# Performance work log

Measured on AMD Instinct MI355X. Metric: run time of the kernel, lower is better.

## Reference

```python
import jax, jax.numpy as jnp
import numpy as np

WS = 7        # window size (cubic)
SHIFT = 3     # shift size (cubic)
NH = 6        # num heads
EPS = 1e-5


def _layernorm(x, g, b):
    m = x.mean(-1, keepdims=True)
    v = ((x - m) ** 2).mean(-1, keepdims=True)
    return (x - m) / jnp.sqrt(v + EPS) * g + b


def _win_partition(x, ws):
    # (B,H,W,T,C) -> (B*nW, ws^3, C)
    B, H, W, T, C = x.shape
    x = x.reshape(B, H // ws, ws, W // ws, ws, T // ws, ws, C)
    return x.transpose(0, 1, 3, 5, 2, 4, 6, 7).reshape(-1, ws * ws * ws, C)


def _win_reverse(w, ws, B, H, W, T):
    # (B*nW, ws^3, C) -> (B,H,W,T,C)
    C = w.shape[-1]
    x = w.reshape(B, H // ws, W // ws, T // ws, ws, ws, ws, C)
    return x.transpose(0, 1, 4, 2, 5, 3, 6, 7).reshape(B, H, W, T, C)


def _rel_index(ws):
    # 3D relative position index, (N, N) int, N = ws^3 (torch.meshgrid default 'ij')
    coords = np.stack(np.meshgrid(np.arange(ws), np.arange(ws), np.arange(ws), indexing='ij'))
    cf = coords.reshape(3, -1)
    rel = (cf[:, :, None] - cf[:, None, :]).transpose(1, 2, 0)
    rel[:, :, 0] += ws - 1
    rel[:, :, 1] += ws - 1
    rel[:, :, 2] += ws - 1
    rel[:, :, 0] *= (2 * ws - 1) ** 2
    rel[:, :, 1] *= (2 * ws - 1)
    return rel.sum(-1)


def _compute_mask(Hp, Wp, Tp, ws, shift):
    img = np.zeros((1, Hp, Wp, Tp, 1), np.float32)
    cnt = 0
    sl = (slice(0, -ws), slice(-ws, -shift), slice(-shift, None))
    for h in sl:
        for w in sl:
            for t in sl:
                img[:, h, w, t, :] = cnt
                cnt += 1
    mw = np.asarray(_win_partition(jnp.asarray(img), ws)).reshape(-1, ws ** 3)  # (nW, N)
    am = mw[:, None, :] - mw[:, :, None]
    return jnp.asarray(np.where(am != 0, -100.0, 0.0).astype(np.float32))


def setup_inputs() -> dict:
    key = jax.random.key(0)
    ks = jax.random.split(key, 10)
    B, Hd, Wd, Td, C = 2, 28, 28, 28, 192
    L = Hd * Wd * Td
    Ch = int(C * 4.0)
    s = 0.02
    inp = {
        'x': jax.random.normal(ks[0], (B, L, C), jnp.float32),
        'mask': _compute_mask(Hd, Wd, Td, WS, SHIFT),
        'gamma1': jnp.ones((C,), jnp.float32),
        'beta1': jnp.zeros((C,), jnp.float32),
        'qkv_w': jax.random.normal(ks[1], (3 * C, C), jnp.float32) * s,
        'qkv_b': jnp.zeros((3 * C,), jnp.float32),
        'rpb_table': jax.random.normal(ks[2], ((2 * WS - 1) ** 3, NH), jnp.float32) * s,
        'proj_w': jax.random.normal(ks[3], (C, C), jnp.float32) * s,
        'proj_b': jnp.zeros((C,), jnp.float32),
        'gamma2': jnp.ones((C,), jnp.float32),
        'beta2': jnp.zeros((C,), jnp.float32),
        'fc1_w': jax.random.normal(ks[4], (Ch, C), jnp.float32) * s,
        'fc1_b': jnp.zeros((Ch,), jnp.float32),
        'fc2_w': jax.random.normal(ks[5], (C, Ch), jnp.float32) * s,
        'fc2_b': jnp.zeros((C,), jnp.float32),
        'H': Hd, 'W': Wd, 'T': Td,
    }
    return inp


def reference(x, mask, gamma1, beta1, qkv_w, qkv_b, rpb_table, proj_w, proj_b,
              gamma2, beta2, fc1_w, fc1_b, fc2_w, fc2_b, H, W, T):
    B, L, C = x.shape
    hd = C // NH
    scale = hd ** -0.5
    shortcut = x

    h1 = _layernorm(x, gamma1, beta1).reshape(B, H, W, T, C)
    # H,W,T are multiples of WS -> no padding; cyclic shift for SW-MSA
    shifted = jnp.roll(h1, (-SHIFT, -SHIFT, -SHIFT), axis=(1, 2, 3))
    xw = _win_partition(shifted, WS)            # (B*nW, N, C)
    Bn, N, _ = xw.shape

    qkv = (xw @ qkv_w.T + qkv_b).reshape(Bn, N, 3, NH, hd).transpose(2, 0, 3, 1, 4)
    q, k, v = qkv[0] * scale, qkv[1], qkv[2]     # (Bn, NH, N, hd)
    attn = jnp.einsum('bhnd,bhmd->bhnm', q, k)   # (Bn, NH, N, N)

    idx = _rel_index(WS)
    bias = rpb_table[idx.reshape(-1)].reshape(N, N, NH).transpose(2, 0, 1)
    attn = attn + bias[None]

    nW = mask.shape[0]
    attn = attn.reshape(Bn // nW, nW, NH, N, N) + mask[None, :, None]
    attn = jax.nn.softmax(attn.reshape(Bn, NH, N, N), axis=-1)

    out = jnp.einsum('bhnm,bhmd->bhnd', attn, v).transpose(0, 2, 1, 3).reshape(Bn, N, C)
    out = out @ proj_w.T + proj_b

    shifted = _win_reverse(out, WS, B, H, W, T)
    xr = jnp.roll(shifted, (SHIFT, SHIFT, SHIFT), axis=(1, 2, 3)).reshape(B, L, C)

    x = shortcut + xr
    h2 = _layernorm(x, gamma2, beta2)
    m = jax.nn.gelu(h2 @ fc1_w.T + fc1_b, approximate=False)
    return x + (m @ fc2_w.T + fc2_b)
```

## Files before the change

### kernel.cpp

```cpp
#include <hip/hip_runtime.h>
#include <hip/hip_bf16.h>

typedef unsigned short u16;
typedef unsigned int u32;
typedef __attribute__((ext_vector_type(8))) short s16x8;
typedef __attribute__((ext_vector_type(4))) float f32x4;

__device__ __forceinline__ u16 f2bf(float f) {
    union { float f; u32 u; } x; x.f = f;
    u32 r = x.u + 0x7fffu + ((x.u >> 16) & 1u);
    return (u16)(r >> 16);
}
__device__ __forceinline__ float bflo(u32 v) {
    union { u32 u; float f; } x; x.u = v << 16; return x.f;
}
__device__ __forceinline__ float bfhi(u32 v) {
    union { u32 u; float f; } x; x.u = v & 0xffff0000u; return x.f;
}
__device__ __forceinline__ u32 cvt_pk_bf16(float a, float b) {
    u32 r;
    asm("v_cvt_pk_bf16_f32 %0, %1, %2" : "=v"(r) : "v"(a), "v"(b));
    return r;
}
__device__ __forceinline__ void gl2lds(const u16* g, u16* l) {
    __builtin_amdgcn_global_load_lds(
        (const __attribute__((address_space(1))) unsigned int*)g,
        (__attribute__((address_space(3))) unsigned int*)l, 16, 0, 0);
}

#define L_TOK 21952
#define C_DIM 192
#define LOG2E 1.4426950408889634f
#define Q2SCALE 0.2550565444463649f
#define BT_STR 352

__global__ __launch_bounds__(256) void cvt_k(const float* __restrict__ s0,
                                             const float* __restrict__ s1,
                                             const float* __restrict__ s2,
                                             const float* __restrict__ s3,
                                             u16* __restrict__ dst)
{
    int i = blockIdx.x * 256 + threadIdx.x;
    float v;
    if (i < 110592) v = s0[i];
    else if (i < 147456) v = s1[i - 110592];
    else if (i < 294912) v = s2[i - 147456];
    else v = s3[i - 294912];
    dst[i] = f2bf(v);
}

__global__ __launch_bounds__(256) void bias48_k(const float* __restrict__ rpb,
                                                u16* __restrict__ biasT)
{
    const int gid = blockIdx.x * 256 + threadIdx.x;
    const int z = gid / 30976;
    const int rem = gid - z * 30976;
    const int m = rem / 88;
    const int n0 = (rem - m * 88) * 4;
    const int hh = z >> 3, wt = z & 7;

    u16 v[4];
    if (m <= 342) {
        const int hm = m / 49, r2 = m - hm * 49, wm = r2 / 7, tm = r2 - wm * 7;
        const int rm = ((wt & 4) ? (hm < 4 ? 1 : 2) : 0) * 9
                     + ((wt & 2) ? (wm < 4 ? 1 : 2) : 0) * 3
                     + ((wt & 1) ? (tm < 4 ? 1 : 2) : 0);
        #pragma unroll
        for (int j = 0; j < 4; j++) {
            const int n = n0 + j;
            float b = -100000.0f;
            if (n <= 342) {
                int hq = n / 49, r1 = n - hq * 49, wq = r1 / 7, tq = r1 - wq * 7;
                int idx = ((hq - hm + 6) * 13 + (wq - wm + 6)) * 13 + (tq - tm + 6);
                b = rpb[idx * 6 + hh];
                int rq = ((wt & 4) ? (hq < 4 ? 1 : 2) : 0) * 9
                       + ((wt & 2) ? (wq < 4 ? 1 : 2) : 0) * 3
                       + ((wt & 1) ? (tq < 4 ? 1 : 2) : 0);
                if (rq != rm) b -= 100.0f;
                b *= LOG2E;
            }
            v[j] = f2bf(b);
        }
    } else {
        const u16 neg = f2bf(-100000.0f);
        v[0] = neg; v[1] = neg; v[2] = neg; v[3] = neg;
    }
    u32 lo = (u32)v[0] | ((u32)v[1] << 16);
    u32 hi = (u32)v[2] | ((u32)v[3] << 16);
    *(uint2*)&biasT[((size_t)z * 352 + m) * BT_STR + n0] = (uint2){lo, hi};
}

template<int MODE>
__global__ __launch_bounds__(256) void ln_k(const float* __restrict__ in,
                                            const float* __restrict__ g,
                                            const float* __restrict__ b,
                                            u16* __restrict__ out)
{
    const int lane = threadIdx.x & 63, wv = threadIdx.x >> 6;
    const int tok = blockIdx.x * 4 + wv;
    size_t base = (size_t)tok * C_DIM;
    float x0 = in[base + lane];
    float x1 = in[base + 64 + lane];
    float x2 = in[base + 128 + lane];
    float s = x0 + x1 + x2;
    float sq = x0 * x0 + x1 * x1 + x2 * x2;
    #pragma unroll
    for (int off = 32; off > 0; off >>= 1) {
        s += __shfl_xor(s, off, 64);
        sq += __shfl_xor(sq, off, 64);
    }
    const float mean = s * (1.0f / 192.0f);
    float var = sq * (1.0f / 192.0f) - mean * mean;
    var = fmaxf(var, 0.0f);
    const float rstd = rsqrtf(var + 1e-5f);

    size_t obase;
    if (MODE == 0) {
        int bi = tok / L_TOK;
        int l = tok - bi * L_TOK;
        int h = l / 784;
        int rm = l - h * 784;
        int w = rm / 28;
        int t = rm - w * 28;
        int hs = h + 25; if (hs >= 28) hs -= 28;
        int ws = w + 25; if (ws >= 28) ws -= 28;
        int ts = t + 25; if (ts >= 28) ts -= 28;
        int win = ((bi * 4 + hs / 7) * 4 + ws / 7) * 4 + ts / 7;
        int n = (hs % 7) * 49 + (ws % 7) * 7 + (ts % 7);
        obase = ((size_t)win * 343 + n) * C_DIM;
    } else {
        obase = base;
    }
    #pragma unroll
    for (int i = 0; i < 3; i++) {
        int c = lane + i * 64;
        float xv = (i == 0) ? x0 : (i == 1) ? x1 : x2;
        float y = (xv - mean) * rstd * g[c] + b[c];
        out[obase + c] = f2bf(y);
    }
}

template<int K, int EPI, int NX>
__global__ __launch_bounds__(256, 8) void gemm64_k(const u16* __restrict__ A,
                                                   const u16* __restrict__ W,
                                                   const float* __restrict__ bias,
                                                   void* __restrict__ outp,
                                                   const void* __restrict__ resp,
                                                   int Ncols)
{
    __shared__ __align__(16) u16 As[2 * 2048];
    __shared__ __align__(16) u16 Bs[2 * 2048];
    const int t = threadIdx.x;
    constexpr int NWG = NX * 686;
    constexpr int QQ = NWG >> 3, RR = NWG & 7;
    const int orig = blockIdx.x;
    const int xcd = orig & 7, rnk = orig >> 3;
    const int wgid = (xcd < RR ? xcd * (QQ + 1) : RR * (QQ + 1) + (xcd - RR) * QQ) + rnk;
    const int bm = wgid / NX;
    const int n0 = (wgid - bm * NX) * 64;

    const int lane = t & 63, wv = t >> 6;
    const int r16 = lane & 15, quad = lane >> 4;
    const int ar = t >> 2, ac = (t & 3) * 8;
    const size_t abase = (size_t)bm * 64 * K;

    f32x4 acc[4];
    #pragma unroll
    for (int fn = 0; fn < 4; fn++) acc[fn] = (f32x4){0.f, 0.f, 0.f, 0.f};

    for (int kc = 0; kc < K; kc += 64) {
        if (kc) __syncthreads();
        #pragma unroll
        for (int kt = 0; kt < 2; kt++) {
            gl2lds(&A[abase + (size_t)ar * K + kc + kt * 32 + ac], &As[kt * 2048 + 8 * t]);
            gl2lds(&W[(size_t)(n0 + ar) * K + kc + kt * 32 + ac], &Bs[kt * 2048 + 8 * t]);
        }
        __syncthreads();
        #pragma unroll
        for (int kt = 0; kt < 2; kt++) {
            s16x8 af = *(const s16x8*)&As[kt * 2048 + (wv * 16 + r16) * 32 + quad * 8];
            #pragma unroll
            for (int fn = 0; fn < 4; fn++) {
                s16x8 bf = *(const s16x8*)&Bs[kt * 2048 + (fn * 16 + r16) * 32 + quad * 8];
                acc[fn] = __builtin_amdgcn_mfma_f32_16x16x32_bf16(af, bf, acc[fn], 0, 0, 0);
            }
        }
    }

    #pragma unroll
    for (int r = 0; r < 4; r++) {
        const int grow = bm * 64 + wv * 16 + quad * 4 + r;
        size_t rowbase = (size_t)grow * ((EPI == 2) ? C_DIM : Ncols);
        #pragma unroll
        for (int fn = 0; fn < 4; fn++) {
            const int gcol = n0 + fn * 16 + r16;
            float v = acc[fn][r] + bias[gcol];
            if (EPI == 0) {
                if (gcol < 192) v *= Q2SCALE;
                ((u16*)outp)[rowbase + gcol] = f2bf(v);
            } else if (EPI == 1) {
                v = 0.5f * v * (1.0f + erff(v * 0.70710678118654752f));
                ((u16*)outp)[rowbase + gcol] = f2bf(v);
            } else {
                size_t o = rowbase + gcol;
                ((float*)outp)[o] = v + ((const float*)resp)[o];
            }
        }
    }
}

__global__ __launch_bounds__(256) void projln_k(const u16* __restrict__ A,
                                                const u16* __restrict__ W,
                                                const float* __restrict__ bias,
                                                const float* __restrict__ res,
                                                const float* __restrict__ g2,
                                                const float* __restrict__ b2,
                                                float* __restrict__ x2,
                                                u16* __restrict__ h2)
{
    constexpr int K = 192;
    __shared__ __align__(16) u16 As[2 * 2048];
    __shared__ __align__(16) u16 Bs[2 * 6144];
    const int t = threadIdx.x, bm = blockIdx.x;
    const int lane = t & 63, wv = t >> 6;
    const int r16 = lane & 15, quad = lane >> 4;
    const int ar = t >> 2, ac = (t & 3) * 8;
    const size_t abase = (size_t)bm * 64 * K;

    f32x4 acc[12];
    #pragma unroll
    for (int fn = 0; fn < 12; fn++) acc[fn] = (f32x4){0.f, 0.f, 0.f, 0.f};

    for (int kc = 0; kc < K; kc += 64) {
        if (kc) __syncthreads();
        #pragma unroll
        for (int kt = 0; kt < 2; kt++) {
            gl2lds(&A[abase + (size_t)ar * K + kc + kt * 32 + ac], &As[kt * 2048 + 8 * t]);
            #pragma unroll
            for (int bb = 0; bb < 3; bb++)
                gl2lds(&W[(size_t)(bb * 64 + ar) * K + kc + kt * 32 + ac],
                       &Bs[kt * 6144 + bb * 2048 + 8 * t]);
        }
        __syncthreads();
        #pragma unroll
        for (int kt = 0; kt < 2; kt++) {
            s16x8 af = *(const s16x8*)&As[kt * 2048 + (wv * 16 + r16) * 32 + quad * 8];
            #pragma unroll
            for (int fn = 0; fn < 12; fn++) {
                s16x8 bf = *(const s16x8*)&Bs[kt * 6144 + (fn * 16 + r16) * 32 + quad * 8];
                acc[fn] = __builtin_amdgcn_mfma_f32_16x16x32_bf16(af, bf, acc[fn], 0, 0, 0);
            }
        }
    }

    #pragma unroll
    for (int r = 0; r < 4; r++) {
        const int grow = bm * 64 + wv * 16 + quad * 4 + r;
        int win = grow / 343, n = grow - win * 343;
        int bi = win >> 6, wi = win & 63;
        int hw = wi >> 4, ww = (wi >> 2) & 3, tw = wi & 3;
        int ph = n / 49, rem = n - ph * 49;
        int pw = rem / 7, pt = rem - pw * 7;
        int h = hw * 7 + ph + 3; if (h >= 28) h -= 28;
        int w = ww * 7 + pw + 3; if (w >= 28) w -= 28;
        int tt = tw * 7 + pt + 3; if (tt >= 28) tt -= 28;
        int l = (h * 28 + w) * 28 + tt;
        size_t rowbase = ((size_t)bi * L_TOK + l) * C_DIM;

        float y[12];
        float s = 0.f, sq = 0.f;
        #pragma unroll
        for (int fn = 0; fn < 12; fn++) {
            const int gcol = fn * 16 + r16;
            float v = acc[fn][r] + bias[gcol] + res[rowbase + gcol];
            y[fn] = v; s += v; sq += v * v;
        }
        #pragma unroll
        for (int off = 1; off < 16; off <<= 1) {
            s += __shfl_xor(s, off, 64);
            sq += __shfl_xor(sq, off, 64);
        }
        const float mean = s * (1.0f / 192.0f);
        float var = sq * (1.0f / 192.0f) - mean * mean;
        var = fmaxf(var, 0.0f);
        const float rstd = rsqrtf(var + 1e-5f);
        #pragma unroll
        for (int fn = 0; fn < 12; fn++) {
            const int gcol = fn * 16 + r16;
            x2[rowbase + gcol] = y[fn];
            h2[rowbase + gcol] = f2bf((y[fn] - mean) * rstd * g2[gcol] + b2[gcol]);
        }
    }
}

__global__ __launch_bounds__(256, 3) void attn_k(const u16* __restrict__ qkv,
                                                 const u16* __restrict__ biasAll,
                                                 u16* __restrict__ out)
{
    __shared__ __align__(16) u16 Ks[352 * 32];
    __shared__ __align__(16) u16 Vt[32 * 360];
    __shared__ __align__(16) u16 Pb[4][16 * 40];

    const int hh = blockIdx.x;
    const int win = blockIdx.y;
    const int wi = win & 63;
    const int t = threadIdx.x, lane = t & 63, wv = t >> 6;
    const int r16 = lane & 15, quad = lane >> 4;
    const size_t qbase = (size_t)win * 343 * 576 + hh * 32;

    for (int j = t; j < 343 * 4; j += 256) {
        int m = j >> 2, ch = j & 3;
        *(uint4*)&Ks[m * 32 + ch * 8] = *(const uint4*)&qkv[qbase + (size_t)m * 576 + 192 + ch * 8];
    }
    if (t < 36) {
        int m = 343 + (t >> 2), ch = t & 3;
        *(uint4*)&Ks[m * 32 + ch * 8] = (uint4){0u, 0u, 0u, 0u};
    }
    for (int i = t; i < 343 * 16; i += 256) {
        int m = i >> 4, d2 = (i & 15) * 2;
        int pm = (m & ~31) + 2 * (m & 15) + ((m >> 4) & 1);
        u32 w2 = *(const u32*)&qkv[qbase + (size_t)m * 576 + 384 + d2];
        Vt[d2 * 360 + pm] = (u16)(w2 & 0xffffu);
        Vt[(d2 + 1) * 360 + pm] = (u16)(w2 >> 16);
    }
    for (int i = t; i < 32 * 9; i += 256) {
        int d = i / 9, m = 343 + i % 9;
        int pm = (m & ~31) + 2 * (m & 15) + ((m >> 4) & 1);
        Vt[d * 360 + pm] = 0;
    }
    __syncthreads();

    const int wt = (((wi >> 4) == 3) ? 4 : 0) | ((((wi >> 2) & 3) == 3) ? 2 : 0)
                 | (((wi & 3) == 3) ? 1 : 0);
    const u16* biashT = biasAll + (size_t)(hh * 8 + wt) * 352 * BT_STR;

    s16x8 onesb;
    #pragma unroll
    for (int j = 0; j < 8; j++) onesb[j] = (short)0x3f80;

    for (int qt = 0; qt < 6; qt++) {
        const int row0 = qt * 64 + wv * 16;
        if (row0 > 342) continue;
        int qrow = row0 + r16; if (qrow > 342) qrow = 342;
        s16x8 qa = *(const s16x8*)&qkv[qbase + (size_t)qrow * 576 + quad * 8];

        const int n0 = row0 + quad * 4;

        f32x4 sacc[22];
        #pragma unroll
        for (int fn = 0; fn < 22; fn++) {
            const int col = fn * 16 + r16;
            uint2 bv = *(const uint2*)&biashT[(size_t)col * BT_STR + n0];
            sacc[fn][0] = bflo(bv.x);
            sacc[fn][1] = bfhi(bv.x);
            sacc[fn][2] = bflo(bv.y);
            sacc[fn][3] = bfhi(bv.y);
        }
        #pragma unroll
        for (int fn = 0; fn < 22; fn++) {
            s16x8 kb = *(const s16x8*)&Ks[(fn * 16 + r16) * 32 + quad * 8];
            sacc[fn] = __builtin_amdgcn_mfma_f32_16x16x32_bf16(qa, kb, sacc[fn], 0, 0, 0);
        }

        #pragma unroll
        for (int fn = 0; fn < 22; fn++) {
            #pragma unroll
            for (int r = 0; r < 4; r++)
                sacc[fn][r] = exp2f(fminf(sacc[fn][r], 42.0f));
        }

        u16* pw = &Pb[wv][0];
        u32* pw32 = (u32*)pw;
        f32x4 oacc0 = (f32x4){0.f, 0.f, 0.f, 0.f};
        f32x4 oacc1 = (f32x4){0.f, 0.f, 0.f, 0.f};
        f32x4 osum  = (f32x4){0.f, 0.f, 0.f, 0.f};
        #pragma unroll
        for (int c = 0; c < 11; c++) {
            asm volatile("s_waitcnt lgkmcnt(0)" ::: "memory");
            #pragma unroll
            for (int r = 0; r < 4; r++)
                pw32[(quad * 4 + r) * 20 + r16] = cvt_pk_bf16(sacc[2 * c][r], sacc[2 * c + 1][r]);
            asm volatile("s_waitcnt lgkmcnt(0)" ::: "memory");
            s16x8 pa = *(const s16x8*)&pw[r16 * 40 + quad * 8];
            s16x8 vb0 = *(const s16x8*)&Vt[r16 * 360 + c * 32 + quad * 8];
            s16x8 vb1 = *(const s16x8*)&Vt[(16 + r16) * 360 + c * 32 + quad * 8];
            oacc0 = __builtin_amdgcn_mfma_f32_16x16x32_bf16(pa, vb0, oacc0, 0, 0, 0);
            oacc1 = __builtin_amdgcn_mfma_f32_16x16x32_bf16(pa, vb1, oacc1, 0, 0, 0);
            osum  = __builtin_amdgcn_mfma_f32_16x16x32_bf16(pa, onesb, osum, 0, 0, 0);
        }

        #pragma unroll
        for (int r = 0; r < 4; r++) {
            const int n = n0 + r;
            if (n < 343) {
                const float rs = osum[r];
                const float inv = rs > 0.0f ? 1.0f / rs : 0.0f;
                size_t o = ((size_t)win * 343 + n) * C_DIM + hh * 32;
                out[o + r16] = f2bf(oacc0[r] * inv);
                out[o + 16 + r16] = f2bf(oacc1[r] * inv);
            }
        }
    }
}

extern "C" void kernel_launch(void* const* d_in, const int* in_sizes, int n_in,
                              void* d_out, int out_size, void* d_ws, size_t ws_size,
                              hipStream_t stream)
{
    const float* x      = (const float*)d_in[0];
    const float* g1     = (const float*)d_in[2];
    const float* b1     = (const float*)d_in[3];
    const float* qkv_w  = (const float*)d_in[4];
    const float* qkv_b  = (const float*)d_in[5];
    const float* rpb    = (const float*)d_in[6];
    const float* proj_w = (const float*)d_in[7];
    const float* proj_b = (const float*)d_in[8];
    const float* g2     = (const float*)d_in[9];
    const float* b2     = (const float*)d_in[10];
    const float* fc1_w  = (const float*)d_in[11];
    const float* fc1_b  = (const float*)d_in[12];
    const float* fc2_w  = (const float*)d_in[13];
    const float* fc2_b  = (const float*)d_in[14];

    char* ws = (char*)d_ws;
    u16* xw        = (u16*)(ws + 0);
    u16* biasT     = (u16*)(ws + 0);
    u16* h2        = (u16*)(ws + 0);
    u16* qkv       = (u16*)(ws + 16861184);
    u16* a1        = (u16*)(ws + 16861184);
    u16* attn_out  = (u16*)(ws + 67444736);
    float* x2      = (float*)(ws + 84305920);
    u16* wbf       = (u16*)(ws + 118028288);
    u16* qkv_wb = wbf;
    u16* proj_wb = wbf + 110592;
    u16* fc1_wb = wbf + 147456;
    u16* fc2_wb = wbf + 294912;

    cvt_k<<<dim3(1728), 256, 0, stream>>>(qkv_w, proj_w, fc1_w, fc2_w, wbf);
    ln_k<0><<<dim3(10976), 256, 0, stream>>>(x, g1, b1, xw);
    gemm64_k<192, 0, 9><<<dim3(9 * 686), 256, 0, stream>>>(xw, qkv_wb, qkv_b, qkv, nullptr, 576);
    bias48_k<<<dim3(5808), 256, 0, stream>>>(rpb, biasT);
    attn_k<<<dim3(6, 128), 256, 0, stream>>>(qkv, biasT, attn_out);
    projln_k<<<dim3(686), 256, 0, stream>>>(attn_out, proj_wb, proj_b, x, g2, b2, x2, h2);
    gemm64_k<192, 1, 12><<<dim3(12 * 686), 256, 0, stream>>>(h2, fc1_wb, fc1_b, a1, nullptr, 768);
    gemm64_k<768, 2, 3><<<dim3(3 * 686), 256, 0, stream>>>(a1, fc2_wb, fc2_b, d_out, x2, 192);
}
```

Measured before the change: 321.5 us.

## Double-buffer LDS staging in GEMM and proj+LN kernels to overlap loads

```diff
diff --git a/kernel.cpp b/kernel.cpp
--- a/kernel.cpp
+++ b/kernel.cpp
@@ -148,8 +148,9 @@
                                                    const void* __restrict__ resp,
                                                    int Ncols)
 {
-    __shared__ __align__(16) u16 As[2 * 2048];
-    __shared__ __align__(16) u16 Bs[2 * 2048];
+    constexpr int NC = K / 64;
+    __shared__ __align__(16) u16 As[2][4096];
+    __shared__ __align__(16) u16 Bs[2][4096];
     const int t = threadIdx.x;
     constexpr int NWG = NX * 686;
     constexpr int QQ = NWG >> 3, RR = NWG & 7;
@@ -168,23 +169,35 @@
     #pragma unroll
     for (int fn = 0; fn < 4; fn++) acc[fn] = (f32x4){0.f, 0.f, 0.f, 0.f};
 
-    for (int kc = 0; kc < K; kc += 64) {
-        if (kc) __syncthreads();
+    auto STAGE = [&](int c, int b) {
         #pragma unroll
         for (int kt = 0; kt < 2; kt++) {
-            gl2lds(&A[abase + (size_t)ar * K + kc + kt * 32 + ac], &As[kt * 2048 + 8 * t]);
-            gl2lds(&W[(size_t)(n0 + ar) * K + kc + kt * 32 + ac], &Bs[kt * 2048 + 8 * t]);
-        }
-        __syncthreads();
+            gl2lds(&A[abase + (size_t)ar * K + c * 64 + kt * 32 + ac], &As[b][kt * 2048 + 8 * t]);
+            gl2lds(&W[(size_t)(n0 + ar) * K + c * 64 + kt * 32 + ac], &Bs[b][kt * 2048 + 8 * t]);
+        }
+    };
+
+    STAGE(0, 0);
+    for (int c = 0; c < NC; ++c) {
+        const int cur = c & 1;
+        if (c + 1 < NC) {
+            STAGE(c + 1, cur ^ 1);
+            asm volatile("s_waitcnt vmcnt(4)" ::: "memory");
+        } else {
+            asm volatile("s_waitcnt vmcnt(0)" ::: "memory");
+        }
+        __builtin_amdgcn_s_barrier();
+        __builtin_amdgcn_sched_barrier(0);
         #pragma unroll
         for (int kt = 0; kt < 2; kt++) {
-            s16x8 af = *(const s16x8*)&As[kt * 2048 + (wv * 16 + r16) * 32 + quad * 8];
+            s16x8 af = *(const s16x8*)&As[cur][kt * 2048 + (wv * 16 + r16) * 32 + quad * 8];
             #pragma unroll
             for (int fn = 0; fn < 4; fn++) {
-                s16x8 bf = *(const s16x8*)&Bs[kt * 2048 + (fn * 16 + r16) * 32 + quad * 8];
+                s16x8 bf = *(const s16x8*)&Bs[cur][kt * 2048 + (fn * 16 + r16) * 32 + quad * 8];
                 acc[fn] = __builtin_amdgcn_mfma_f32_16x16x32_bf16(af, bf, acc[fn], 0, 0, 0);
             }
         }
+        __builtin_amdgcn_s_barrier();
     }
 
     #pragma unroll
@@ -218,9 +231,9 @@
                                                 float* __restrict__ x2,
                                                 u16* __restrict__ h2)
 {
-    constexpr int K = 192;
-    __shared__ __align__(16) u16 As[2 * 2048];
-    __shared__ __align__(16) u16 Bs[2 * 6144];
+    constexpr int K = 192, NC = 3;
+    __shared__ __align__(16) u16 As[2][4096];
+    __shared__ __align__(16) u16 Bs[2][12288];
     const int t = threadIdx.x, bm = blockIdx.x;
     const int lane = t & 63, wv = t >> 6;
     const int r16 = lane & 15, quad = lane >> 4;
@@ -231,26 +244,38 @@
     #pragma unroll
     for (int fn = 0; fn < 12; fn++) acc[fn] = (f32x4){0.f, 0.f, 0.f, 0.f};
 
-    for (int kc = 0; kc < K; kc += 64) {
-        if (kc) __syncthreads();
+    auto STAGE = [&](int c, int b) {
         #pragma unroll
         for (int kt = 0; kt < 2; kt++) {
-            gl2lds(&A[abase + (size_t)ar * K + kc + kt * 32 + ac], &As[kt * 2048 + 8 * t]);
+            gl2lds(&A[abase + (size_t)ar * K + c * 64 + kt * 32 + ac], &As[b][kt * 2048 + 8 * t]);
             #pragma unroll
             for (int bb = 0; bb < 3; bb++)
-                gl2lds(&W[(size_t)(bb * 64 + ar) * K + kc + kt * 32 + ac],
-                       &Bs[kt * 6144 + bb * 2048 + 8 * t]);
-        }
-        __syncthreads();
+                gl2lds(&W[(size_t)(bb * 64 + ar) * K + c * 64 + kt * 32 + ac],
+                       &Bs[b][kt * 6144 + bb * 2048 + 8 * t]);
+        }
+    };
+
+    STAGE(0, 0);
+    for (int c = 0; c < NC; ++c) {
+        const int cur = c & 1;
+        if (c + 1 < NC) {
+            STAGE(c + 1, cur ^ 1);
+            asm volatile("s_waitcnt vmcnt(8)" ::: "memory");
+        } else {
+            asm volatile("s_waitcnt vmcnt(0)" ::: "memory");
+        }
+        __builtin_amdgcn_s_barrier();
+        __builtin_amdgcn_sched_barrier(0);
         #pragma unroll
         for (int kt = 0; kt < 2; kt++) {
-            s16x8 af = *(const s16x8*)&As[kt * 2048 + (wv * 16 + r16) * 32 + quad * 8];
+            s16x8 af = *(const s16x8*)&As[cur][kt * 2048 + (wv * 16 + r16) * 32 + quad * 8];
             #pragma unroll
             for (int fn = 0; fn < 12; fn++) {
-                s16x8 bf = *(const s16x8*)&Bs[kt * 6144 + (fn * 16 + r16) * 32 + quad * 8];
+                s16x8 bf = *(const s16x8*)&Bs[cur][kt * 6144 + (fn * 16 + r16) * 32 + quad * 8];
                 acc[fn] = __builtin_amdgcn_mfma_f32_16x16x32_bf16(af, bf, acc[fn], 0, 0, 0);
             }
         }
+        __builtin_amdgcn_s_barrier();
     }
 
     #pragma unroll
```

Result: no change. 320.1 us (-0.5%).
